# Optimization experiments

Hardware: AMD Instinct MI355X
Metric: run time of the kernel (lower is better)

## Reference

```python
import jax, jax.numpy as jnp
import numpy as np

S, B, D = 2048, 32, 1024  # seq_len, batch, in_dim; out_dim = 2*D

def setup_inputs() -> dict:
    key = jax.random.key(0)
    k1, k2, k3, k4 = jax.random.split(key, 4)
    return {
        "input": jax.random.normal(k1, (S, B, D), dtype=jnp.float32),
        "h": jax.random.normal(k2, (B, D), dtype=jnp.float32),
        "Wi": jax.random.normal(k3, (D, D), dtype=jnp.float32) * 0.02,
        "Wo": jax.random.normal(k4, (D, 2 * D), dtype=jnp.float32) * 0.02,
    }

def reference(input, h, Wi, Wo):
    # semi = Wi(h), broadcast over seq dim (torch expand_as)
    semi = h @ Wi.T                                   # [B, D]
    # score logits: elementwise mult + sum over feature dim
    logits = jnp.einsum('sbd,bd->bs', input, semi)    # [B, S]
    # legacy nn.Softmax() on 2D tensor normalizes over dim=1 (= seq)
    attn = jax.nn.softmax(logits, axis=1)             # [B, S]
    # weighted sum over sequence
    s_tilde = jnp.einsum('bs,sbd->bd', attn, input)   # [B, D]
    # output projection + tanh
    c_t = jnp.tanh(jnp.concatenate([s_tilde, h], axis=1) @ Wo.T)  # [B, D]
    return c_t
```

## Files before the change

kernel.cpp:

```cpp
#include <hip/hip_runtime.h>
#include <math.h>

#define S_LEN   2048
#define BATCH   32
#define DIM     1024
#define P_CHUNKS 32
#define CHUNK   (S_LEN / P_CHUNKS)

__global__ __launch_bounds__(256) void gemm_skinny(
    const float* __restrict__ A, const float* __restrict__ W,
    float* __restrict__ out, int K, int Dout, int act)
{
    __shared__ __align__(16) float At[32 * 256];

    const int t    = threadIdx.x;
    const int lane = t & 63;
    const int wid  = t >> 6;
    const int d    = blockIdx.x * 4 + wid;

    float acc[32];
#pragma unroll
    for (int b = 0; b < 32; ++b) acc[b] = 0.0f;

    for (int k0 = 0; k0 < K; k0 += 256) {
#pragma unroll
        for (int i = 0; i < 8; ++i) {
            int f4id = t + i * 256;
            int bb   = f4id >> 6;
            int c4   = f4id & 63;
            ((float4*)At)[bb * 64 + c4] =
                ((const float4*)(A + (size_t)bb * K + k0))[c4];
        }
        __syncthreads();

        float4 w4 = ((const float4*)(W + (size_t)d * K + k0))[lane];

#pragma unroll
        for (int b = 0; b < 32; ++b) {
            float4 a4 = ((const float4*)At)[b * 64 + lane];
            acc[b] = fmaf(w4.x, a4.x, acc[b]);
            acc[b] = fmaf(w4.y, a4.y, acc[b]);
            acc[b] = fmaf(w4.z, a4.z, acc[b]);
            acc[b] = fmaf(w4.w, a4.w, acc[b]);
        }
        __syncthreads();
    }

    float mine = 0.0f;
#pragma unroll
    for (int b = 0; b < 32; ++b) {
        float v = acc[b];
#pragma unroll
        for (int off = 32; off > 0; off >>= 1) v += __shfl_xor(v, off, 64);
        if (lane == b) mine = v;
    }
    if (lane < 32) {
        float o = act ? tanhf(mine) : mine;
        out[(size_t)lane * Dout + d] = o;
    }
}

__global__ __launch_bounds__(256) void attn_partial(
    const float* __restrict__ input, const float* __restrict__ semi,
    float* __restrict__ pacc, float* __restrict__ pm, float* __restrict__ pl)
{
    const int p  = blockIdx.x;
    const int b  = blockIdx.y;
    const int t  = threadIdx.x;
    const int lane = t & 63;
    const int wid  = t >> 6;
    const int s0 = p * CHUNK;

    __shared__ float red[2][4];

    const float4 sm4 = ((const float4*)(semi + (size_t)b * DIM))[t];
    const float4* rp =
        (const float4*)(input + ((size_t)s0 * BATCH + b) * DIM) + t;
    const int rstride = BATCH * DIM / 4;

    float m = -INFINITY, l = 0.0f;
    float4 acc = make_float4(0.f, 0.f, 0.f, 0.f);

    float4 xn = *rp;
    for (int i = 0; i < CHUNK; ++i) {
        float4 x = xn;
        if (i + 1 < CHUNK) xn = rp[(i + 1) * rstride];

        float pd = x.x * sm4.x + x.y * sm4.y + x.z * sm4.z + x.w * sm4.w;
#pragma unroll
        for (int off = 32; off > 0; off >>= 1) pd += __shfl_xor(pd, off, 64);
        if (lane == 0) red[i & 1][wid] = pd;
        __syncthreads();
        float logit = red[i & 1][0] + red[i & 1][1]
                    + red[i & 1][2] + red[i & 1][3];

        float mn = fmaxf(m, logit);
        float sc = __expf(m - mn);
        float f  = __expf(logit - mn);
        acc.x = fmaf(f, x.x, acc.x * sc);
        acc.y = fmaf(f, x.y, acc.y * sc);
        acc.z = fmaf(f, x.z, acc.z * sc);
        acc.w = fmaf(f, x.w, acc.w * sc);
        l = fmaf(l, sc, f);
        m = mn;
    }

    ((float4*)(pacc + ((size_t)b * P_CHUNKS + p) * DIM))[t] = acc;
    if (t == 0) {
        pm[b * P_CHUNKS + p] = m;
        pl[b * P_CHUNKS + p] = l;
    }
}

__global__ __launch_bounds__(256) void combine(
    const float* __restrict__ pacc, const float* __restrict__ pm,
    const float* __restrict__ pl, const float* __restrict__ h,
    float* __restrict__ cat)
{
    const int b = blockIdx.x;
    const int q = blockIdx.y;
    const int t = threadIdx.x;

    __shared__ float fsc[32];
    __shared__ float smv[32], slv[32];
    __shared__ float Linv;

    if (t < 32) {
        smv[t] = pm[b * P_CHUNKS + t];
        slv[t] = pl[b * P_CHUNKS + t];
    }
    __syncthreads();
    if (t == 0) {
        float M = -INFINITY;
        for (int pp = 0; pp < 32; ++pp) M = fmaxf(M, smv[pp]);
        float L = 0.0f;
        for (int pp = 0; pp < 32; ++pp) {
            float f = __expf(smv[pp] - M);
            fsc[pp] = f;
            L = fmaf(slv[pp], f, L);
        }
        Linv = 1.0f / L;
    }
    __syncthreads();

    const int d = q * 256 + t;
    float sum = 0.0f;
#pragma unroll
    for (int pp = 0; pp < 32; ++pp)
        sum = fmaf(fsc[pp], pacc[((size_t)b * P_CHUNKS + pp) * DIM + d], sum);

    cat[(size_t)b * (2 * DIM) + d]       = sum * Linv;
    cat[(size_t)b * (2 * DIM) + DIM + d] = h[(size_t)b * DIM + d];
}

extern "C" void kernel_launch(void* const* d_in, const int* in_sizes, int n_in,
                              void* d_out, int out_size, void* d_ws, size_t ws_size,
                              hipStream_t stream)
{
    const float* input = (const float*)d_in[0];
    const float* h     = (const float*)d_in[1];
    const float* Wi    = (const float*)d_in[2];
    const float* Wo    = (const float*)d_in[3];
    float* out = (float*)d_out;

    float* ws   = (float*)d_ws;
    float* semi = ws;
    float* pacc = semi + 32 * 1024;
    float* pm   = pacc + 32 * 32 * 1024;
    float* pl   = pm + 1024;
    float* cat  = pl + 1024;

    hipLaunchKernelGGL(gemm_skinny, dim3(256), dim3(256), 0, stream,
                       h, Wi, semi, 1024, 1024, 0);
    hipLaunchKernelGGL(attn_partial, dim3(P_CHUNKS, BATCH), dim3(256), 0, stream,
                       input, semi, pacc, pm, pl);
    hipLaunchKernelGGL(combine, dim3(BATCH, 4), dim3(256), 0, stream,
                       pacc, pm, pl, h, cat);
    hipLaunchKernelGGL(gemm_skinny, dim3(256), dim3(256), 0, stream,
                       cat, Wo, out, 2048, 1024, 1);
}
```

Measured before the change: 419.4 us.

## Split attention chunks per wave and double-buffer skinny GEMM loads

The attention partial kernel now gives each wave its own sub-chunk of rows with a full-row dot product held in registers. This removes the per-row __syncthreads and shared-memory reduction, at the cost of four times as many partial results (128 per batch) for the combine step. The combine kernel does its max and sum with wave-wide reductions and accumulates in four independent chains. The skinny GEMM double-buffers the A tile in shared memory and prefetches A and W into registers, dropping one barrier per iteration. The larger partial buffer raises workspace traffic and size.

```diff
diff --git a/kernel.cpp b/kernel.cpp
--- a/kernel.cpp
+++ b/kernel.cpp
@@ -1,17 +1,19 @@
 #include <hip/hip_runtime.h>
 #include <math.h>
 
-#define S_LEN   2048
-#define BATCH   32
-#define DIM     1024
+#define S_LEN    2048
+#define BATCH    32
+#define DIM      1024
 #define P_CHUNKS 32
-#define CHUNK   (S_LEN / P_CHUNKS)
+#define CHUNK    (S_LEN / P_CHUNKS)
+#define ROWS_PER_WAVE (CHUNK / 4)
+#define NPART    (P_CHUNKS * 4)
 
 __global__ __launch_bounds__(256) void gemm_skinny(
     const float* __restrict__ A, const float* __restrict__ W,
     float* __restrict__ out, int K, int Dout, int act)
 {
-    __shared__ __align__(16) float At[32 * 256];
+    __shared__ __align__(16) float At[2][32 * 256];
 
     const int t    = threadIdx.x;
     const int lane = t & 63;
@@ -22,28 +24,49 @@
 #pragma unroll
     for (int b = 0; b < 32; ++b) acc[b] = 0.0f;
 
+    float4 sreg[8];
+#pragma unroll
+    for (int i = 0; i < 8; ++i) {
+        int f4id = t + i * 256;
+        int bb   = f4id >> 6;
+        int c4   = f4id & 63;
+        sreg[i] = ((const float4*)(A + (size_t)bb * K))[c4];
+    }
+    float4 w4 = ((const float4*)(W + (size_t)d * K))[lane];
+
+    int buf = 0;
     for (int k0 = 0; k0 < K; k0 += 256) {
 #pragma unroll
         for (int i = 0; i < 8; ++i) {
             int f4id = t + i * 256;
             int bb   = f4id >> 6;
             int c4   = f4id & 63;
-            ((float4*)At)[bb * 64 + c4] =
-                ((const float4*)(A + (size_t)bb * K + k0))[c4];
+            ((float4*)At[buf])[bb * 64 + c4] = sreg[i];
         }
         __syncthreads();
 
-        float4 w4 = ((const float4*)(W + (size_t)d * K + k0))[lane];
+        float4 w4c = w4;
+        if (k0 + 256 < K) {
+            const int k1 = k0 + 256;
+#pragma unroll
+            for (int i = 0; i < 8; ++i) {
+                int f4id = t + i * 256;
+                int bb   = f4id >> 6;
+                int c4   = f4id & 63;
+                sreg[i] = ((const float4*)(A + (size_t)bb * K + k1))[c4];
+            }
+            w4 = ((const float4*)(W + (size_t)d * K + k1))[lane];
+        }
 
 #pragma unroll
         for (int b = 0; b < 32; ++b) {
-            float4 a4 = ((const float4*)At)[b * 64 + lane];
-            acc[b] = fmaf(w4.x, a4.x, acc[b]);
-            acc[b] = fmaf(w4.y, a4.y, acc[b]);
-            acc[b] = fmaf(w4.z, a4.z, acc[b]);
-            acc[b] = fmaf(w4.w, a4.w, acc[b]);
-        }
-        __syncthreads();
+            float4 a4 = ((const float4*)At[buf])[b * 64 + lane];
+            acc[b] = fmaf(w4c.x, a4.x, acc[b]);
+            acc[b] = fmaf(w4c.y, a4.y, acc[b]);
+            acc[b] = fmaf(w4c.z, a4.z, acc[b]);
+            acc[b] = fmaf(w4c.w, a4.w, acc[b]);
+        }
+        buf ^= 1;
     }
 
     float mine = 0.0f;
@@ -64,51 +87,73 @@
     const float* __restrict__ input, const float* __restrict__ semi,
     float* __restrict__ pacc, float* __restrict__ pm, float* __restrict__ pl)
 {
-    const int p  = blockIdx.x;
-    const int b  = blockIdx.y;
-    const int t  = threadIdx.x;
+    const int p    = blockIdx.x;
+    const int b    = blockIdx.y;
+    const int t    = threadIdx.x;
     const int lane = t & 63;
-    const int wid  = t >> 6;
-    const int s0 = p * CHUNK;
-
-    __shared__ float red[2][4];
-
-    const float4 sm4 = ((const float4*)(semi + (size_t)b * DIM))[t];
-    const float4* rp =
-        (const float4*)(input + ((size_t)s0 * BATCH + b) * DIM) + t;
-    const int rstride = BATCH * DIM / 4;
+    const int w    = t >> 6;
+    const int part = p * 4 + w;
+    const int s0   = p * CHUNK + w * ROWS_PER_WAVE;
+
+    const float4* sp = (const float4*)(semi + (size_t)b * DIM);
+    const float4 sm0 = sp[lane];
+    const float4 sm1 = sp[lane + 64];
+    const float4 sm2 = sp[lane + 128];
+    const float4 sm3 = sp[lane + 192];
+
+    const float4* rp = (const float4*)(input + ((size_t)s0 * BATCH + b) * DIM);
+    const size_t rstride = (size_t)BATCH * DIM / 4;
 
     float m = -INFINITY, l = 0.0f;
-    float4 acc = make_float4(0.f, 0.f, 0.f, 0.f);
-
-    float4 xn = *rp;
-    for (int i = 0; i < CHUNK; ++i) {
-        float4 x = xn;
-        if (i + 1 < CHUNK) xn = rp[(i + 1) * rstride];
-
-        float pd = x.x * sm4.x + x.y * sm4.y + x.z * sm4.z + x.w * sm4.w;
+    float4 a0 = make_float4(0.f, 0.f, 0.f, 0.f);
+    float4 a1 = a0, a2 = a0, a3 = a0;
+
+    float4 x0 = rp[lane], x1 = rp[lane + 64], x2 = rp[lane + 128], x3 = rp[lane + 192];
+
+#pragma unroll 1
+    for (int j = 0; j < ROWS_PER_WAVE; ++j) {
+        const float4 c0 = x0, c1 = x1, c2 = x2, c3 = x3;
+        if (j + 1 < ROWS_PER_WAVE) {
+            const float4* np = rp + (size_t)(j + 1) * rstride;
+            x0 = np[lane];       x1 = np[lane + 64];
+            x2 = np[lane + 128]; x3 = np[lane + 192];
+        }
+
+        float pd = c0.x * sm0.x;
+        pd = fmaf(c0.y, sm0.y, pd); pd = fmaf(c0.z, sm0.z, pd); pd = fmaf(c0.w, sm0.w, pd);
+        pd = fmaf(c1.x, sm1.x, pd); pd = fmaf(c1.y, sm1.y, pd);
+        pd = fmaf(c1.z, sm1.z, pd); pd = fmaf(c1.w, sm1.w, pd);
+        pd = fmaf(c2.x, sm2.x, pd); pd = fmaf(c2.y, sm2.y, pd);
+        pd = fmaf(c2.z, sm2.z, pd); pd = fmaf(c2.w, sm2.w, pd);
+        pd = fmaf(c3.x, sm3.x, pd); pd = fmaf(c3.y, sm3.y, pd);
+        pd = fmaf(c3.z, sm3.z, pd); pd = fmaf(c3.w, sm3.w, pd);
+
 #pragma unroll
         for (int off = 32; off > 0; off >>= 1) pd += __shfl_xor(pd, off, 64);
-        if (lane == 0) red[i & 1][wid] = pd;
-        __syncthreads();
-        float logit = red[i & 1][0] + red[i & 1][1]
-                    + red[i & 1][2] + red[i & 1][3];
-
-        float mn = fmaxf(m, logit);
-        float sc = __expf(m - mn);
-        float f  = __expf(logit - mn);
-        acc.x = fmaf(f, x.x, acc.x * sc);
-        acc.y = fmaf(f, x.y, acc.y * sc);
-        acc.z = fmaf(f, x.z, acc.z * sc);
-        acc.w = fmaf(f, x.w, acc.w * sc);
+
+        const float mn = fmaxf(m, pd);
+        const float sc = __expf(m - mn);
+        const float f  = __expf(pd - mn);
+        a0.x = fmaf(f, c0.x, a0.x * sc); a0.y = fmaf(f, c0.y, a0.y * sc);
+        a0.z = fmaf(f, c0.z, a0.z * sc); a0.w = fmaf(f, c0.w, a0.w * sc);
+        a1.x = fmaf(f, c1.x, a1.x * sc); a1.y = fmaf(f, c1.y, a1.y * sc);
+        a1.z = fmaf(f, c1.z, a1.z * sc); a1.w = fmaf(f, c1.w, a1.w * sc);
+        a2.x = fmaf(f, c2.x, a2.x * sc); a2.y = fmaf(f, c2.y, a2.y * sc);
+        a2.z = fmaf(f, c2.z, a2.z * sc); a2.w = fmaf(f, c2.w, a2.w * sc);
+        a3.x = fmaf(f, c3.x, a3.x * sc); a3.y = fmaf(f, c3.y, a3.y * sc);
+        a3.z = fmaf(f, c3.z, a3.z * sc); a3.w = fmaf(f, c3.w, a3.w * sc);
         l = fmaf(l, sc, f);
         m = mn;
     }
 
-    ((float4*)(pacc + ((size_t)b * P_CHUNKS + p) * DIM))[t] = acc;
-    if (t == 0) {
-        pm[b * P_CHUNKS + p] = m;
-        pl[b * P_CHUNKS + p] = l;
+    float4* op = (float4*)(pacc + ((size_t)b * NPART + part) * DIM);
+    op[lane]       = a0;
+    op[lane + 64]  = a1;
+    op[lane + 128] = a2;
+    op[lane + 192] = a3;
+    if (lane == 0) {
+        pm[b * NPART + part] = m;
+        pl[b * NPART + part] = l;
     }
 }
 
@@ -121,33 +166,43 @@
     const int q = blockIdx.y;
     const int t = threadIdx.x;
 
-    __shared__ float fsc[32];
-    __shared__ float smv[32], slv[32];
+    __shared__ float fsc[NPART];
+    __shared__ float smv[NPART], slv[NPART];
     __shared__ float Linv;
 
-    if (t < 32) {
-        smv[t] = pm[b * P_CHUNKS + t];
-        slv[t] = pl[b * P_CHUNKS + t];
+    if (t < NPART) {
+        smv[t] = pm[b * NPART + t];
+        slv[t] = pl[b * NPART + t];
     }
     __syncthreads();
-    if (t == 0) {
-        float M = -INFINITY;
-        for (int pp = 0; pp < 32; ++pp) M = fmaxf(M, smv[pp]);
-        float L = 0.0f;
-        for (int pp = 0; pp < 32; ++pp) {
-            float f = __expf(smv[pp] - M);
-            fsc[pp] = f;
-            L = fmaf(slv[pp], f, L);
-        }
-        Linv = 1.0f / L;
+
+    if (t < 64) {
+        const float m0 = smv[t], m1 = smv[t + 64];
+        float mx = fmaxf(m0, m1);
+#pragma unroll
+        for (int off = 32; off > 0; off >>= 1) mx = fmaxf(mx, __shfl_xor(mx, off, 64));
+        const float f0 = __expf(m0 - mx);
+        const float f1 = __expf(m1 - mx);
+        fsc[t]      = f0;
+        fsc[t + 64] = f1;
+        float L = fmaf(slv[t], f0, slv[t + 64] * f1);
+#pragma unroll
+        for (int off = 32; off > 0; off >>= 1) L += __shfl_xor(L, off, 64);
+        if (t == 0) Linv = 1.0f / L;
     }
     __syncthreads();
 
     const int d = q * 256 + t;
-    float sum = 0.0f;
-#pragma unroll
-    for (int pp = 0; pp < 32; ++pp)
-        sum = fmaf(fsc[pp], pacc[((size_t)b * P_CHUNKS + pp) * DIM + d], sum);
+    const float* pb = pacc + (size_t)b * NPART * DIM + d;
+    float s0 = 0.f, s1 = 0.f, s2 = 0.f, s3 = 0.f;
+#pragma unroll
+    for (int pp = 0; pp < NPART; pp += 4) {
+        s0 = fmaf(fsc[pp + 0], pb[(size_t)(pp + 0) * DIM], s0);
+        s1 = fmaf(fsc[pp + 1], pb[(size_t)(pp + 1) * DIM], s1);
+        s2 = fmaf(fsc[pp + 2], pb[(size_t)(pp + 2) * DIM], s2);
+        s3 = fmaf(fsc[pp + 3], pb[(size_t)(pp + 3) * DIM], s3);
+    }
+    const float sum = (s0 + s1) + (s2 + s3);
 
     cat[(size_t)b * (2 * DIM) + d]       = sum * Linv;
     cat[(size_t)b * (2 * DIM) + DIM + d] = h[(size_t)b * DIM + d];
@@ -166,9 +221,9 @@
     float* ws   = (float*)d_ws;
     float* semi = ws;
     float* pacc = semi + 32 * 1024;
-    float* pm   = pacc + 32 * 32 * 1024;
-    float* pl   = pm + 1024;
-    float* cat  = pl + 1024;
+    float* pm   = pacc + (size_t)32 * NPART * 1024;
+    float* pl   = pm + 32 * NPART;
+    float* cat  = pl + 32 * NPART;
 
     hipLaunchKernelGGL(gemm_skinny, dim3(256), dim3(256), 0, stream,
                        h, Wi, semi, 1024, 1024, 0);
```

Measured after the change: 415.8 us. Within noise of the previous version (-0.8%).
